# Kernel optimization log

Hardware: AMD Instinct MI355X
Metric: run time of the kernel (lower is better)

The kernel has to match this reference:

```python
import jax, jax.numpy as jnp
import numpy as np

DIM = 1024
HEADS = 16
HD = DIM // HEADS            # 64
MLP = 4 * DIM                # 4096
IN_OUT = MLP + 3 * DIM       # 7168, in_proj out dim
OUT_IN = MLP + DIM           # 5120, out_proj in dim
OUT_OUT = 2 * DIM            # 2048, out_proj out dim
R = 2                        # residual PQ levels
K = 64                       # codebook size
NCB = HEADS                  # num_codebooks = num_heads * codebooks_ratio
IN_CLUSTERS = HEADS * (IN_OUT // DIM)                 # 112
OUT_CLUSTERS = HEADS * max(1, OUT_OUT // OUT_IN)      # 16
SUB_IN = DIM // NCB          # 64
SUB_OUT = OUT_IN // NCB      # 320
EPS = 1e-5


def setup_inputs() -> dict:
    key = jax.random.key(0)
    k1, k2, k3, k4, k5 = jax.random.split(key, 5)
    B, N = 4, 1024
    x = jax.random.normal(k1, (B, N, DIM), jnp.float32)
    in_codebooks = jax.random.normal(k2, (R, IN_CLUSTERS, NCB, K, SUB_IN), jnp.float32) * 0.02
    in_indices = jax.random.randint(k3, (R, IN_OUT, NCB), 0, K, jnp.int32)
    out_codebooks = jax.random.normal(k4, (R, OUT_CLUSTERS, NCB, K, SUB_OUT), jnp.float32) * 0.02
    out_indices = jax.random.randint(k5, (R, OUT_OUT, NCB), 0, K, jnp.int32)
    return {"x": x, "in_codebooks": in_codebooks, "in_indices": in_indices,
            "out_codebooks": out_codebooks, "out_indices": out_indices}


def _decode_weight(cb, idx):
    """Decode RPQ weight. cb: (R, n_clusters, n_codebooks, K, sub), idx: (R, O, n_codebooks).
    Returns dense weight (O, n_codebooks*sub)."""
    Rr, nclust, C, _, sub = cb.shape
    O = idx.shape[1]
    cluster = jnp.arange(O) // (O // nclust)                       # per-row cluster id
    w = cb[jnp.arange(Rr)[:, None, None],
           cluster[None, :, None],
           jnp.arange(C)[None, None, :],
           idx]                                                    # (R, O, C, sub)
    return w.sum(0).reshape(O, C * sub)


def reference(x, in_codebooks, in_indices, out_codebooks, out_indices):
    B, N, C = x.shape
    res = x
    # LayerNorm without affine
    mu = x.mean(-1, keepdims=True)
    var = x.var(-1, keepdims=True)
    xn = (x - mu) * jax.lax.rsqrt(var + EPS)
    # in_proj: dequant + GEMM
    Win = _decode_weight(in_codebooks, in_indices)                 # (IN_OUT, DIM)
    h = jnp.einsum('bnc,oc->bno', xn, Win)                         # (B, N, IN_OUT)
    xm, q, k, v = jnp.split(h, [MLP, MLP + DIM, MLP + 2 * DIM], axis=-1)
    q = q.reshape(B, N, HEADS, HD).transpose(0, 2, 1, 3)
    k = k.reshape(B, N, HEADS, HD).transpose(0, 2, 1, 3)
    v = v.reshape(B, N, HEADS, HD).transpose(0, 2, 1, 3)
    scale = HD ** -0.5
    attn = jax.nn.softmax(jnp.einsum('bhqd,bhkd->bhqk', q, k) * scale, axis=-1)
    xa = jnp.einsum('bhqk,bhkd->bhqd', attn, v).transpose(0, 2, 1, 3).reshape(B, N, C)
    # out_proj: dequant + GEMM on concatenated [mlp, attn]
    Wout = _decode_weight(out_codebooks, out_indices)              # (OUT_OUT, OUT_IN)
    o = jnp.einsum('bnc,oc->bno', jnp.concatenate([xm, xa], axis=-1), Wout)
    x_mlp, x_attn = o[..., :DIM], o[..., DIM:]
    return x_mlp + x_attn + res
```

## Files before the change

kernel.cpp:

```cpp
#include <hip/hip_runtime.h>
#include <hip/hip_bf16.h>

typedef float f32x4 __attribute__((ext_vector_type(4)));
typedef short short8 __attribute__((ext_vector_type(8)));

#define LDH 7168
#define MFMA16(d, x, y) d = __builtin_amdgcn_mfma_f32_16x16x32_bf16(x, y, d, 0, 0, 0)

__device__ __forceinline__ void async_ld16(const void* g, void* l) {
  __builtin_amdgcn_global_load_lds(
      (const __attribute__((address_space(1))) unsigned int*)g,
      (__attribute__((address_space(3))) unsigned int*)l, 16, 0, 0);
}

__device__ __forceinline__ float bf2f(unsigned short u) {
  union { unsigned int i; float f; } c; c.i = ((unsigned int)u) << 16; return c.f;
}

__device__ __forceinline__ ushort4 pack_bf16x4(float4 v) {
  ushort4 u;
  __hip_bfloat16 b;
  b = __float2bfloat16(v.x); u.x = *(unsigned short*)&b;
  b = __float2bfloat16(v.y); u.y = *(unsigned short*)&b;
  b = __float2bfloat16(v.z); u.z = *(unsigned short*)&b;
  b = __float2bfloat16(v.w); u.w = *(unsigned short*)&b;
  return u;
}

__global__ __launch_bounds__(256) void decode_win_k(const float* __restrict__ cb,
                                                    const int* __restrict__ idx,
                                                    __hip_bfloat16* __restrict__ Win) {
  const int o = blockIdx.x;
  const int cluster = o >> 6;
  const int c = threadIdx.x >> 4;
  const int s4 = (threadIdx.x & 15) * 4;
  const int k0 = idx[o * 16 + c];
  const int k1 = idx[(7168 + o) * 16 + c];
  const float4 v0 = *(const float4*)&cb[((((size_t)cluster) * 16 + c) * 64 + k0) * 64 + s4];
  const float4 v1 = *(const float4*)&cb[((((size_t)(112 + cluster)) * 16 + c) * 64 + k1) * 64 + s4];
  float4 v; v.x = v0.x + v1.x; v.y = v0.y + v1.y; v.z = v0.z + v1.z; v.w = v0.w + v1.w;
  *(ushort4*)&Win[(size_t)o * 1024 + c * 64 + s4] = pack_bf16x4(v);
}

__global__ __launch_bounds__(256) void decode_weff_k(const float* __restrict__ cb,
                                                     const int* __restrict__ idx,
                                                     __hip_bfloat16* __restrict__ W) {
  const int o = blockIdx.x;
  const int cl1 = o >> 7, cl2 = cl1 + 8;
  for (int e4 = threadIdx.x * 4; e4 < 5120; e4 += 1024) {
    const int c = e4 / 320, s = e4 - c * 320;
    float4 acc = {0.f, 0.f, 0.f, 0.f};
    #pragma unroll
    for (int r = 0; r < 2; ++r) {
      const int ka = idx[((size_t)r * 2048 + o) * 16 + c];
      const int kb = idx[((size_t)r * 2048 + o + 1024) * 16 + c];
      const float4 va = *(const float4*)&cb[((((size_t)r * 16 + cl1) * 16 + c) * 64 + ka) * 320 + s];
      const float4 vb = *(const float4*)&cb[((((size_t)r * 16 + cl2) * 16 + c) * 64 + kb) * 320 + s];
      acc.x += va.x + vb.x; acc.y += va.y + vb.y; acc.z += va.z + vb.z; acc.w += va.w + vb.w;
    }
    *(ushort4*)&W[(size_t)o * 5120 + e4] = pack_bf16x4(acc);
  }
}

__global__ __launch_bounds__(256) void ln_k(const float* __restrict__ x,
                                            __hip_bfloat16* __restrict__ xn) {
  const int row = blockIdx.x;
  const float4 v = ((const float4*)(x + (size_t)row * 1024))[threadIdx.x];
  float s = v.x + v.y + v.z + v.w;
  float s2 = v.x * v.x + v.y * v.y + v.z * v.z + v.w * v.w;
  #pragma unroll
  for (int off = 32; off > 0; off >>= 1) {
    s += __shfl_down(s, off, 64);
    s2 += __shfl_down(s2, off, 64);
  }
  __shared__ float red[8];
  if ((threadIdx.x & 63) == 0) { red[threadIdx.x >> 6] = s; red[4 + (threadIdx.x >> 6)] = s2; }
  __syncthreads();
  s = red[0] + red[1] + red[2] + red[3];
  s2 = red[4] + red[5] + red[6] + red[7];
  const float mu = s * (1.f / 1024.f);
  const float rstd = rsqrtf(s2 * (1.f / 1024.f) - mu * mu + 1e-5f);
  float4 nv;
  nv.x = (v.x - mu) * rstd; nv.y = (v.y - mu) * rstd;
  nv.z = (v.z - mu) * rstd; nv.w = (v.w - mu) * rstd;
  *(ushort4*)(xn + (size_t)row * 1024 + threadIdx.x * 4) = pack_bf16x4(nv);
}

__global__ __launch_bounds__(512, 2) void gemm1_k(const __hip_bfloat16* __restrict__ A,
                                                  const __hip_bfloat16* __restrict__ B,
                                                  __hip_bfloat16* __restrict__ C,
                                                  __hip_bfloat16* __restrict__ vT) {
  __shared__ ushort sm[65536];
  const int tid = threadIdx.x;
  const int lane = tid & 63, wid = tid >> 6;
  const int g = lane >> 4, r16 = lane & 15;
  const int wr = wid >> 2, wc = wid & 3;

  const int x = blockIdx.x & 7, local = blockIdx.x >> 3;
  const int mb = (x >> 1) * 4 + local / 14;
  const int nb = (x & 1) * 14 + local % 14;
  const int m0 = mb * 256, n0 = nb * 256;

  auto stageA = [&](int kt, int base) {
    #pragma unroll
    for (int i = 0; i < 4; ++i) {
      const int c = i * 512 + tid;
      const int lc = c ^ (((c >> 5) & 1) << 1);
      const int row = lc >> 3, col = (lc & 7) * 8;
      async_ld16(&A[(size_t)(m0 + row) * 1024 + kt * 64 + col], &sm[base + c * 8]);
    }
  };
  auto stageB = [&](int kt, int base) {
    #pragma unroll
    for (int i = 0; i < 4; ++i) {
      const int c = i * 512 + tid;
      const int lc = c ^ (((c >> 5) & 1) << 1);
      const int row = lc >> 3, col = (lc & 7) * 8;
      async_ld16(&B[(size_t)(n0 + row) * 1024 + kt * 64 + col], &sm[base + 16384 + c * 8]);
    }
  };
  auto rdA = [&](int base, int mm, int kk) -> short8 {
    const int row = wr * 128 + mm * 16 + r16;
    int e = row * 64 + kk * 32 + g * 8;
    e ^= ((row >> 2) & 1) << 4;
    return *(const short8*)&sm[base + e];
  };
  auto rdB = [&](int base, int nn, int kk) -> short8 {
    const int row = wc * 64 + nn * 16 + r16;
    int e = row * 64 + kk * 32 + g * 8;
    e ^= ((row >> 2) & 1) << 4;
    return *(const short8*)&sm[base + 16384 + e];
  };

  f32x4 acc[8][4] = {};

  stageA(0, 0); stageB(0, 0);
  asm volatile("s_waitcnt vmcnt(0)" ::: "memory");
  __builtin_amdgcn_s_barrier();
  __builtin_amdgcn_sched_barrier(0);

  auto tile_body = [&](int kt, int base, int nbase) {
    short8 a0[4][2], a1[4][2], b0[2][2], b1[2][2];
    #pragma unroll
    for (int mm = 0; mm < 4; ++mm) { a0[mm][0] = rdA(base, mm, 0); a0[mm][1] = rdA(base, mm, 1); }
    #pragma unroll
    for (int nn = 0; nn < 2; ++nn) { b0[nn][0] = rdB(base, nn, 0); b0[nn][1] = rdB(base, nn, 1); }
    if (kt + 1 < 16) stageA(kt + 1, nbase);
    __builtin_amdgcn_s_setprio(1);
    #pragma unroll
    for (int mm = 0; mm < 4; ++mm)
      #pragma unroll
      for (int nn = 0; nn < 2; ++nn) {
        MFMA16(acc[mm][nn], a0[mm][0], b0[nn][0]);
        MFMA16(acc[mm][nn], a0[mm][1], b0[nn][1]);
      }
    __builtin_amdgcn_s_setprio(0);
    __builtin_amdgcn_s_barrier();
    #pragma unroll
    for (int nn = 0; nn < 2; ++nn) { b1[nn][0] = rdB(base, 2 + nn, 0); b1[nn][1] = rdB(base, 2 + nn, 1); }
    if (kt + 1 < 16) stageB(kt + 1, nbase);
    __builtin_amdgcn_s_setprio(1);
    #pragma unroll
    for (int mm = 0; mm < 4; ++mm)
      #pragma unroll
      for (int nn = 0; nn < 2; ++nn) {
        MFMA16(acc[mm][2 + nn], a0[mm][0], b1[nn][0]);
        MFMA16(acc[mm][2 + nn], a0[mm][1], b1[nn][1]);
      }
    __builtin_amdgcn_s_setprio(0);
    __builtin_amdgcn_s_barrier();
    #pragma unroll
    for (int mm = 0; mm < 4; ++mm) { a1[mm][0] = rdA(base, 4 + mm, 0); a1[mm][1] = rdA(base, 4 + mm, 1); }
    __builtin_amdgcn_s_setprio(1);
    #pragma unroll
    for (int mm = 0; mm < 4; ++mm)
      #pragma unroll
      for (int nn = 0; nn < 2; ++nn) {
        MFMA16(acc[4 + mm][2 + nn], a1[mm][0], b1[nn][0]);
        MFMA16(acc[4 + mm][2 + nn], a1[mm][1], b1[nn][1]);
      }
    __builtin_amdgcn_s_setprio(0);
    __builtin_amdgcn_s_barrier();
    __builtin_amdgcn_s_setprio(1);
    #pragma unroll
    for (int mm = 0; mm < 4; ++mm)
      #pragma unroll
      for (int nn = 0; nn < 2; ++nn) {
        MFMA16(acc[4 + mm][nn], a1[mm][0], b0[nn][0]);
        MFMA16(acc[4 + mm][nn], a1[mm][1], b0[nn][1]);
      }
    __builtin_amdgcn_s_setprio(0);
    asm volatile("s_waitcnt vmcnt(0) lgkmcnt(0)" ::: "memory");
    __builtin_amdgcn_s_barrier();
    __builtin_amdgcn_sched_barrier(0);
  };

  for (int kt = 0; kt < 16; kt += 2) {
    tile_body(kt, 0, 32768);
    tile_body(kt + 1, 32768, 0);
  }

  if (n0 < 6144) {
    #pragma unroll
    for (int mm = 0; mm < 8; ++mm)
      #pragma unroll
      for (int nn = 0; nn < 4; ++nn)
        #pragma unroll
        for (int r = 0; r < 4; ++r) {
          const int m = m0 + wr * 128 + mm * 16 + g * 4 + r;
          const int o = n0 + wc * 64 + nn * 16 + r16;
          C[(size_t)m * LDH + o] = __float2bfloat16(acc[mm][nn][r]);
        }
  } else {
    #pragma unroll
    for (int mm = 0; mm < 8; ++mm)
      #pragma unroll
      for (int nn = 0; nn < 4; ++nn)
        #pragma unroll
        for (int r = 0; r < 4; ++r) {
          const int m = m0 + wr * 128 + mm * 16 + g * 4 + r;
          const int o = n0 + wc * 64 + nn * 16 + r16;
          const int b_ = m >> 10;
          vT[((size_t)b_ * 1024 + (o - 6144)) * 1024 + (m & 1023)] = __float2bfloat16(acc[mm][nn][r]);
        }
  }
}

__global__ __launch_bounds__(256) void attn_k(const __hip_bfloat16* __restrict__ h,
                                              const __hip_bfloat16* __restrict__ vT,
                                              __hip_bfloat16* __restrict__ xa) {
  const int qt = blockIdx.x, head = blockIdx.y, b = blockIdx.z;
  const int tid = threadIdx.x;
  const int lane = tid & 63, w = tid >> 6;
  const int g = lane >> 4, r16 = lane & 15;

  __shared__ __align__(16) __hip_bfloat16 Ks[2][64 * 64];
  __shared__ __align__(16) __hip_bfloat16 Vs[2][64 * 64];
  __shared__ __align__(16) __hip_bfloat16 P[4][16][72];

  const __hip_bfloat16* Kg = h + (size_t)(b * 1024) * LDH + 5120 + head * 64;
  const __hip_bfloat16* Vg = vT + ((size_t)b * 1024 + head * 64) * 1024;

  const size_t qrow = (size_t)(b * 1024 + qt * 64 + w * 16 + r16);
  short8 aq0 = *(const short8*)&h[qrow * LDH + 4096 + head * 64 + g * 8];
  short8 aq1 = *(const short8*)&h[qrow * LDH + 4096 + head * 64 + 32 + g * 8];

  auto stage = [&](int buf, int t) {
    #pragma unroll
    for (int i = 0; i < 2; ++i) {
      const int c_lin = i * 256 + tid;
      const int row = c_lin >> 3;
      const int c_log = (c_lin & 7) ^ (row & 7);
      async_ld16(&Kg[(size_t)(t * 64 + row) * LDH + c_log * 8], &Ks[buf][c_lin * 8]);
    }
    #pragma unroll
    for (int i = 0; i < 2; ++i) {
      const int c_lin = i * 256 + tid;
      const int row = c_lin >> 3;
      const int c_log = (c_lin & 7) ^ (row & 7);
      async_ld16(&Vg[(size_t)row * 1024 + t * 64 + c_log * 8], &Vs[buf][c_lin * 8]);
    }
  };

  f32x4 o_acc[4] = {};
  float m_r[4], l_r[4];
  #pragma unroll
  for (int r = 0; r < 4; ++r) { m_r[r] = -1e30f; l_r[r] = 0.f; }

  stage(0, 0);
  for (int t = 0; t < 16; ++t) {
    const int buf = t & 1;
    if (t + 1 < 16) {
      stage(buf ^ 1, t + 1);
      asm volatile("s_waitcnt vmcnt(4)" ::: "memory");
    } else {
      asm volatile("s_waitcnt vmcnt(0)" ::: "memory");
    }
    __builtin_amdgcn_s_barrier();
    __builtin_amdgcn_sched_barrier(0);

    f32x4 s_acc[4] = {};
    #pragma unroll
    for (int nn = 0; nn < 4; ++nn) {
      const int row = nn * 16 + r16;
      short8 bk0 = *(const short8*)&Ks[buf][row * 64 + ((g ^ (row & 7)) * 8)];
      short8 bk1 = *(const short8*)&Ks[buf][row * 64 + (((g + 4) ^ (row & 7)) * 8)];
      s_acc[nn] = __builtin_amdgcn_mfma_f32_16x16x32_bf16(aq0, bk0, s_acc[nn], 0, 0, 0);
      s_acc[nn] = __builtin_amdgcn_mfma_f32_16x16x32_bf16(aq1, bk1, s_acc[nn], 0, 0, 0);
    }
    #pragma unroll
    for (int nn = 0; nn < 4; ++nn) s_acc[nn] *= 0.125f;

    #pragma unroll
    for (int r = 0; r < 4; ++r) {
      float mx = fmaxf(fmaxf(s_acc[0][r], s_acc[1][r]), fmaxf(s_acc[2][r], s_acc[3][r]));
      #pragma unroll
      for (int off = 1; off < 16; off <<= 1) mx = fmaxf(mx, __shfl_xor(mx, off, 64));
      const float mn = fmaxf(m_r[r], mx);
      const float al = __expf(m_r[r] - mn);
      m_r[r] = mn;
      float ps = 0.f;
      #pragma unroll
      for (int nn = 0; nn < 4; ++nn) {
        const float p = __expf(s_acc[nn][r] - mn);
        s_acc[nn][r] = p;
        ps += p;
      }
      #pragma unroll
      for (int off = 1; off < 16; off <<= 1) ps += __shfl_xor(ps, off, 64);
      l_r[r] = l_r[r] * al + ps;
      o_acc[0][r] *= al; o_acc[1][r] *= al; o_acc[2][r] *= al; o_acc[3][r] *= al;
    }

    #pragma unroll
    for (int nn = 0; nn < 4; ++nn)
      #pragma unroll
      for (int r = 0; r < 4; ++r)
        P[w][g * 4 + r][nn * 16 + r16] = __float2bfloat16(s_acc[nn][r]);
    short8 ap0 = *(const short8*)&P[w][r16][g * 8];
    short8 ap1 = *(const short8*)&P[w][r16][32 + g * 8];

    #pragma unroll
    for (int nn = 0; nn < 4; ++nn) {
      const int row = nn * 16 + r16;
      short8 bv0 = *(const short8*)&Vs[buf][row * 64 + ((g ^ (row & 7)) * 8)];
      short8 bv1 = *(const short8*)&Vs[buf][row * 64 + (((g + 4) ^ (row & 7)) * 8)];
      o_acc[nn] = __builtin_amdgcn_mfma_f32_16x16x32_bf16(ap0, bv0, o_acc[nn], 0, 0, 0);
      o_acc[nn] = __builtin_amdgcn_mfma_f32_16x16x32_bf16(ap1, bv1, o_acc[nn], 0, 0, 0);
    }
    __builtin_amdgcn_s_barrier();
    __builtin_amdgcn_sched_barrier(0);
  }

  #pragma unroll
  for (int r = 0; r < 4; ++r) {
    const float inv = 1.0f / l_r[r];
    const size_t mrow = (size_t)(b * 1024 + qt * 64 + w * 16 + g * 4 + r);
    #pragma unroll
    for (int nn = 0; nn < 4; ++nn)
      xa[mrow * 1024 + head * 64 + nn * 16 + r16] = __float2bfloat16(o_acc[nn][r] * inv);
  }
}

__global__ __launch_bounds__(512, 2) void gemm2_k(const __hip_bfloat16* __restrict__ h,
                                                  const __hip_bfloat16* __restrict__ xa,
                                                  const __hip_bfloat16* __restrict__ W,
                                                  __hip_bfloat16* __restrict__ p0,
                                                  __hip_bfloat16* __restrict__ p1,
                                                  __hip_bfloat16* __restrict__ p2,
                                                  float* __restrict__ out) {
  __shared__ ushort sm[65536];
  const int tid = threadIdx.x;
  const int lane = tid & 63, wid = tid >> 6;
  const int g = lane >> 4, r16 = lane & 15;
  const int wr = wid >> 2, wc = wid & 3;

  int bid = blockIdx.x;
  bid = (bid & 7) * 8 + (bid >> 3);
  const int mb = bid >> 2, nb = bid & 3;
  const int m0 = mb * 256, n0 = nb * 256;
  const int z = blockIdx.y;
  const int kt0 = z * 20, ktEnd = kt0 + 20;

  auto stageA = [&](int kt, int base) {
    const __hip_bfloat16* Ab; size_t lda; int kc;
    if (kt < 64) { Ab = h;  lda = LDH;  kc = kt * 64; }
    else         { Ab = xa; lda = 1024; kc = kt * 64 - 4096; }
    #pragma unroll
    for (int i = 0; i < 4; ++i) {
      const int c = i * 512 + tid;
      const int lc = c ^ (((c >> 5) & 1) << 1);
      const int row = lc >> 3, col = (lc & 7) * 8;
      async_ld16(&Ab[(size_t)(m0 + row) * lda + kc + col], &sm[base + c * 8]);
    }
  };
  auto stageB = [&](int kt, int base) {
    #pragma unroll
    for (int i = 0; i < 4; ++i) {
      const int c = i * 512 + tid;
      const int lc = c ^ (((c >> 5) & 1) << 1);
      const int row = lc >> 3, col = (lc & 7) * 8;
      async_ld16(&W[(size_t)(n0 + row) * 5120 + kt * 64 + col], &sm[base + 16384 + c * 8]);
    }
  };
  auto rdA = [&](int base, int mm, int kk) -> short8 {
    const int row = wr * 128 + mm * 16 + r16;
    int e = row * 64 + kk * 32 + g * 8;
    e ^= ((row >> 2) & 1) << 4;
    return *(const short8*)&sm[base + e];
  };
  auto rdB = [&](int base, int nn, int kk) -> short8 {
    const int row = wc * 64 + nn * 16 + r16;
    int e = row * 64 + kk * 32 + g * 8;
    e ^= ((row >> 2) & 1) << 4;
    return *(const short8*)&sm[base + 16384 + e];
  };

  f32x4 acc[8][4] = {};

  stageA(kt0, 0); stageB(kt0, 0);
  asm volatile("s_waitcnt vmcnt(0)" ::: "memory");
  __builtin_amdgcn_s_barrier();
  __builtin_amdgcn_sched_barrier(0);

  auto tile_body = [&](int kt, int base, int nbase) {
    short8 a0[4][2], a1[4][2], b0[2][2], b1[2][2];
    #pragma unroll
    for (int mm = 0; mm < 4; ++mm) { a0[mm][0] = rdA(base, mm, 0); a0[mm][1] = rdA(base, mm, 1); }
    #pragma unroll
    for (int nn = 0; nn < 2; ++nn) { b0[nn][0] = rdB(base, nn, 0); b0[nn][1] = rdB(base, nn, 1); }
    if (kt + 1 < ktEnd) stageA(kt + 1, nbase);
    __builtin_amdgcn_s_setprio(1);
    #pragma unroll
    for (int mm = 0; mm < 4; ++mm)
      #pragma unroll
      for (int nn = 0; nn < 2; ++nn) {
        MFMA16(acc[mm][nn], a0[mm][0], b0[nn][0]);
        MFMA16(acc[mm][nn], a0[mm][1], b0[nn][1]);
      }
    __builtin_amdgcn_s_setprio(0);
    __builtin_amdgcn_s_barrier();
    #pragma unroll
    for (int nn = 0; nn < 2; ++nn) { b1[nn][0] = rdB(base, 2 + nn, 0); b1[nn][1] = rdB(base, 2 + nn, 1); }
    if (kt + 1 < ktEnd) stageB(kt + 1, nbase);
    __builtin_amdgcn_s_setprio(1);
    #pragma unroll
    for (int mm = 0; mm < 4; ++mm)
      #pragma unroll
      for (int nn = 0; nn < 2; ++nn) {
        MFMA16(acc[mm][2 + nn], a0[mm][0], b1[nn][0]);
        MFMA16(acc[mm][2 + nn], a0[mm][1], b1[nn][1]);
      }
    __builtin_amdgcn_s_setprio(0);
    __builtin_amdgcn_s_barrier();
    #pragma unroll
    for (int mm = 0; mm < 4; ++mm) { a1[mm][0] = rdA(base, 4 + mm, 0); a1[mm][1] = rdA(base, 4 + mm, 1); }
    __builtin_amdgcn_s_setprio(1);
    #pragma unroll
    for (int mm = 0; mm < 4; ++mm)
      #pragma unroll
      for (int nn = 0; nn < 2; ++nn) {
        MFMA16(acc[4 + mm][2 + nn], a1[mm][0], b1[nn][0]);
        MFMA16(acc[4 + mm][2 + nn], a1[mm][1], b1[nn][1]);
      }
    __builtin_amdgcn_s_setprio(0);
    __builtin_amdgcn_s_barrier();
    __builtin_amdgcn_s_setprio(1);
    #pragma unroll
    for (int mm = 0; mm < 4; ++mm)
      #pragma unroll
      for (int nn = 0; nn < 2; ++nn) {
        MFMA16(acc[4 + mm][nn], a1[mm][0], b0[nn][0]);
        MFMA16(acc[4 + mm][nn], a1[mm][1], b0[nn][1]);
      }
    __builtin_amdgcn_s_setprio(0);
    asm volatile("s_waitcnt vmcnt(0) lgkmcnt(0)" ::: "memory");
    __builtin_amdgcn_s_barrier();
    __builtin_amdgcn_sched_barrier(0);
  };

  for (int kt = kt0; kt < ktEnd; kt += 2) {
    tile_body(kt, 0, 32768);
    tile_body(kt + 1, 32768, 0);
  }

  __hip_bfloat16* pz = (z == 0) ? p0 : (z == 1) ? p1 : p2;
  #pragma unroll
  for (int mm = 0; mm < 8; ++mm)
    #pragma unroll
    for (int nn = 0; nn < 4; ++nn)
      #pragma unroll
      for (int r = 0; r < 4; ++r) {
        const int m = m0 + wr * 128 + mm * 16 + g * 4 + r;
        const int n = n0 + wc * 64 + nn * 16 + r16;
        if (z == 3) out[(size_t)m * 1024 + n] = acc[mm][nn][r];
        else        pz[(size_t)m * 1024 + n] = __float2bfloat16(acc[mm][nn][r]);
      }
}

__global__ __launch_bounds__(256) void reduce_k(const __hip_bfloat16* __restrict__ p0,
                                                const __hip_bfloat16* __restrict__ p1,
                                                const __hip_bfloat16* __restrict__ p2,
                                                const float* __restrict__ res,
                                                float* __restrict__ out) {
  const size_t i4 = (size_t)blockIdx.x * 256 + threadIdx.x;
  float4 o = ((const float4*)out)[i4];
  const float4 rr = ((const float4*)res)[i4];
  const ushort4 a0 = ((const ushort4*)p0)[i4];
  const ushort4 a1 = ((const ushort4*)p1)[i4];
  const ushort4 a2 = ((const ushort4*)p2)[i4];
  o.x += rr.x + bf2f(a0.x) + bf2f(a1.x) + bf2f(a2.x);
  o.y += rr.y + bf2f(a0.y) + bf2f(a1.y) + bf2f(a2.y);
  o.z += rr.z + bf2f(a0.z) + bf2f(a1.z) + bf2f(a2.z);
  o.w += rr.w + bf2f(a0.w) + bf2f(a1.w) + bf2f(a2.w);
  ((float4*)out)[i4] = o;
}

extern "C" void kernel_launch(void* const* d_in, const int* in_sizes, int n_in,
                              void* d_out, int out_size, void* d_ws, size_t ws_size,
                              hipStream_t stream) {
  (void)in_sizes; (void)n_in; (void)out_size; (void)ws_size;
  const float* x      = (const float*)d_in[0];
  const float* in_cb  = (const float*)d_in[1];
  const int*   in_idx = (const int*)d_in[2];
  const float* out_cb = (const float*)d_in[3];
  const int*   out_idx= (const int*)d_in[4];
  float* out = (float*)d_out;
  char* ws = (char*)d_ws;

  __hip_bfloat16* Win  = (__hip_bfloat16*)(ws);
  __hip_bfloat16* Weff = (__hip_bfloat16*)(ws + 14680064);
  __hip_bfloat16* xn   = (__hip_bfloat16*)(ws + 25165824);
  __hip_bfloat16* h    = (__hip_bfloat16*)(ws + 33554432);
  __hip_bfloat16* vT   = (__hip_bfloat16*)(ws + 92274688);
  __hip_bfloat16* xa   = (__hip_bfloat16*)(ws + 100663296);

  __hip_bfloat16* pk0 = Win;
  __hip_bfloat16* pk1 = xn;
  __hip_bfloat16* pk2 = vT;

  decode_win_k<<<dim3(7168), dim3(256), 0, stream>>>(in_cb, in_idx, Win);
  decode_weff_k<<<dim3(1024), dim3(256), 0, stream>>>(out_cb, out_idx, Weff);
  ln_k<<<dim3(4096), dim3(256), 0, stream>>>(x, xn);
  gemm1_k<<<dim3(448), dim3(512), 0, stream>>>(xn, Win, h, vT);
  attn_k<<<dim3(16, 16, 4), dim3(256), 0, stream>>>(h, vT, xa);
  gemm2_k<<<dim3(64, 4), dim3(512), 0, stream>>>(h, xa, Weff, pk0, pk1, pk2, out);
  reduce_k<<<dim3(4096), dim3(256), 0, stream>>>(pk0, pk1, pk2, x, out);
}
```

Measured before the change: 219.2 us.

## Deepen GEMM prefetch to two tiles ahead with split half-tile async loads

Measured after the change: 220.7 us. Within noise of the previous version (+0.7%).

```diff
diff --git a/kernel.cpp b/kernel.cpp
--- a/kernel.cpp
+++ b/kernel.cpp
@@ -101,22 +101,22 @@
   const int nb = (x & 1) * 14 + local % 14;
   const int m0 = mb * 256, n0 = nb * 256;
 
-  auto stageA = [&](int kt, int base) {
-    #pragma unroll
-    for (int i = 0; i < 4; ++i) {
-      const int c = i * 512 + tid;
+  auto stA = [&](int tt, int hf) {
+    #pragma unroll
+    for (int i = 0; i < 2; ++i) {
+      const int c = hf * 1024 + i * 512 + tid;
       const int lc = c ^ (((c >> 5) & 1) << 1);
       const int row = lc >> 3, col = (lc & 7) * 8;
-      async_ld16(&A[(size_t)(m0 + row) * 1024 + kt * 64 + col], &sm[base + c * 8]);
-    }
-  };
-  auto stageB = [&](int kt, int base) {
-    #pragma unroll
-    for (int i = 0; i < 4; ++i) {
-      const int c = i * 512 + tid;
+      async_ld16(&A[(size_t)(m0 + row) * 1024 + tt * 64 + col], &sm[(tt & 1) * 32768 + c * 8]);
+    }
+  };
+  auto stB = [&](int tt, int hf) {
+    #pragma unroll
+    for (int i = 0; i < 2; ++i) {
+      const int c = hf * 1024 + i * 512 + tid;
       const int lc = c ^ (((c >> 5) & 1) << 1);
       const int row = lc >> 3, col = (lc & 7) * 8;
-      async_ld16(&B[(size_t)(n0 + row) * 1024 + kt * 64 + col], &sm[base + 16384 + c * 8]);
+      async_ld16(&B[(size_t)(n0 + row) * 1024 + tt * 64 + col], &sm[(tt & 1) * 32768 + 16384 + c * 8]);
     }
   };
   auto rdA = [&](int base, int mm, int kk) -> short8 {
@@ -134,18 +134,21 @@
 
   f32x4 acc[8][4] = {};
 
-  stageA(0, 0); stageB(0, 0);
-  asm volatile("s_waitcnt vmcnt(0)" ::: "memory");
+  stA(0, 0); stA(0, 1); stB(0, 0); stB(0, 1);
+  stA(1, 0); stA(1, 1); stB(1, 0); stB(1, 1);
+  asm volatile("s_waitcnt vmcnt(8)" ::: "memory");
   __builtin_amdgcn_s_barrier();
   __builtin_amdgcn_sched_barrier(0);
 
-  auto tile_body = [&](int kt, int base, int nbase) {
+  #pragma unroll 2
+  for (int t = 0; t < 16; ++t) {
+    const int base = (t & 1) * 32768;
     short8 a0[4][2], a1[4][2], b0[2][2], b1[2][2];
     #pragma unroll
     for (int mm = 0; mm < 4; ++mm) { a0[mm][0] = rdA(base, mm, 0); a0[mm][1] = rdA(base, mm, 1); }
     #pragma unroll
     for (int nn = 0; nn < 2; ++nn) { b0[nn][0] = rdB(base, nn, 0); b0[nn][1] = rdB(base, nn, 1); }
-    if (kt + 1 < 16) stageA(kt + 1, nbase);
+    if (t >= 1 && t + 1 < 16) stA(t + 1, 1);
     __builtin_amdgcn_s_setprio(1);
     #pragma unroll
     for (int mm = 0; mm < 4; ++mm)
@@ -156,9 +159,9 @@
       }
     __builtin_amdgcn_s_setprio(0);
     __builtin_amdgcn_s_barrier();
+    __builtin_amdgcn_sched_barrier(0);
     #pragma unroll
     for (int nn = 0; nn < 2; ++nn) { b1[nn][0] = rdB(base, 2 + nn, 0); b1[nn][1] = rdB(base, 2 + nn, 1); }
-    if (kt + 1 < 16) stageB(kt + 1, nbase);
     __builtin_amdgcn_s_setprio(1);
     #pragma unroll
     for (int mm = 0; mm < 4; ++mm)
@@ -169,8 +172,10 @@
       }
     __builtin_amdgcn_s_setprio(0);
     __builtin_amdgcn_s_barrier();
+    __builtin_amdgcn_sched_barrier(0);
     #pragma unroll
     for (int mm = 0; mm < 4; ++mm) { a1[mm][0] = rdA(base, 4 + mm, 0); a1[mm][1] = rdA(base, 4 + mm, 1); }
+    if (t + 2 < 16) stB(t + 2, 0);
     __builtin_amdgcn_s_setprio(1);
     #pragma unroll
     for (int mm = 0; mm < 4; ++mm)
@@ -181,6 +186,8 @@
       }
     __builtin_amdgcn_s_setprio(0);
     __builtin_amdgcn_s_barrier();
+    __builtin_amdgcn_sched_barrier(0);
+    if (t + 2 < 16) { stB(t + 2, 1); stA(t + 2, 0); }
     __builtin_amdgcn_s_setprio(1);
     #pragma unroll
     for (int mm = 0; mm < 4; ++mm)
@@ -190,14 +197,10 @@
         MFMA16(acc[4 + mm][nn], a1[mm][1], b0[nn][1]);
       }
     __builtin_amdgcn_s_setprio(0);
-    asm volatile("s_waitcnt vmcnt(0) lgkmcnt(0)" ::: "memory");
-    __builtin_amdgcn_s_barrier();
-    __builtin_amdgcn_sched_barrier(0);
-  };
-
-  for (int kt = 0; kt < 16; kt += 2) {
-    tile_body(kt, 0, 32768);
-    tile_body(kt + 1, 32768, 0);
+    if (t + 2 < 16) asm volatile("s_waitcnt vmcnt(6)" ::: "memory");
+    else            asm volatile("s_waitcnt vmcnt(0)" ::: "memory");
+    __builtin_amdgcn_s_barrier();
+    __builtin_amdgcn_sched_barrier(0);
   }
 
   if (n0 < 6144) {
@@ -342,7 +345,7 @@
   }
 }
 
-__global__ __launch_bounds__(512, 2) void gemm2_k(const __hip_bfloat16* __restrict__ h,
+__global__ __launch_bounds__(512, 2) void gemm2_k(const __hip_bfloat16* __restrict__ hbuf,
                                                   const __hip_bfloat16* __restrict__ xa,
                                                   const __hip_bfloat16* __restrict__ W,
                                                   __hip_bfloat16* __restrict__ p0,
@@ -360,27 +363,29 @@
   const int mb = bid >> 2, nb = bid & 3;
   const int m0 = mb * 256, n0 = nb * 256;
   const int z = blockIdx.y;
-  const int kt0 = z * 20, ktEnd = kt0 + 20;
-
-  auto stageA = [&](int kt, int base) {
+  const int kt0 = z * 20;
+
+  auto stA = [&](int lt, int hf) {
+    const int gt = kt0 + lt;
     const __hip_bfloat16* Ab; size_t lda; int kc;
-    if (kt < 64) { Ab = h;  lda = LDH;  kc = kt * 64; }
-    else         { Ab = xa; lda = 1024; kc = kt * 64 - 4096; }
-    #pragma unroll
-    for (int i = 0; i < 4; ++i) {
-      const int c = i * 512 + tid;
+    if (gt < 64) { Ab = hbuf; lda = LDH;  kc = gt * 64; }
+    else         { Ab = xa;   lda = 1024; kc = gt * 64 - 4096; }
+    #pragma unroll
+    for (int i = 0; i < 2; ++i) {
+      const int c = hf * 1024 + i * 512 + tid;
       const int lc = c ^ (((c >> 5) & 1) << 1);
       const int row = lc >> 3, col = (lc & 7) * 8;
-      async_ld16(&Ab[(size_t)(m0 + row) * lda + kc + col], &sm[base + c * 8]);
-    }
-  };
-  auto stageB = [&](int kt, int base) {
-    #pragma unroll
-    for (int i = 0; i < 4; ++i) {
-      const int c = i * 512 + tid;
+      async_ld16(&Ab[(size_t)(m0 + row) * lda + kc + col], &sm[(lt & 1) * 32768 + c * 8]);
+    }
+  };
+  auto stB = [&](int lt, int hf) {
+    const int gt = kt0 + lt;
+    #pragma unroll
+    for (int i = 0; i < 2; ++i) {
+      const int c = hf * 1024 + i * 512 + tid;
       const int lc = c ^ (((c >> 5) & 1) << 1);
       const int row = lc >> 3, col = (lc & 7) * 8;
-      async_ld16(&W[(size_t)(n0 + row) * 5120 + kt * 64 + col], &sm[base + 16384 + c * 8]);
+      async_ld16(&W[(size_t)(n0 + row) * 5120 + gt * 64 + col], &sm[(lt & 1) * 32768 + 16384 + c * 8]);
     }
   };
   auto rdA = [&](int base, int mm, int kk) -> short8 {
@@ -398,18 +403,21 @@
 
   f32x4 acc[8][4] = {};
 
-  stageA(kt0, 0); stageB(kt0, 0);
-  asm volatile("s_waitcnt vmcnt(0)" ::: "memory");
+  stA(0, 0); stA(0, 1); stB(0, 0); stB(0, 1);
+  stA(1, 0); stA(1, 1); stB(1, 0); stB(1, 1);
+  asm volatile("s_waitcnt vmcnt(8)" ::: "memory");
   __builtin_amdgcn_s_barrier();
   __builtin_amdgcn_sched_barrier(0);
 
-  auto tile_body = [&](int kt, int base, int nbase) {
+  #pragma unroll 2
+  for (int t = 0; t < 20; ++t) {
+    const int base = (t & 1) * 32768;
     short8 a0[4][2], a1[4][2], b0[2][2], b1[2][2];
     #pragma unroll
     for (int mm = 0; mm < 4; ++mm) { a0[mm][0] = rdA(base, mm, 0); a0[mm][1] = rdA(base, mm, 1); }
     #pragma unroll
     for (int nn = 0; nn < 2; ++nn) { b0[nn][0] = rdB(base, nn, 0); b0[nn][1] = rdB(base, nn, 1); }
-    if (kt + 1 < ktEnd) stageA(kt + 1, nbase);
+    if (t >= 1 && t + 1 < 20) stA(t + 1, 1);
     __builtin_amdgcn_s_setprio(1);
     #pragma unroll
     for (int mm = 0; mm < 4; ++mm)
@@ -420,9 +428,9 @@
       }
     __builtin_amdgcn_s_setprio(0);
     __builtin_amdgcn_s_barrier();
+    __builtin_amdgcn_sched_barrier(0);
     #pragma unroll
     for (int nn = 0; nn < 2; ++nn) { b1[nn][0] = rdB(base, 2 + nn, 0); b1[nn][1] = rdB(base, 2 + nn, 1); }
-    if (kt + 1 < ktEnd) stageB(kt + 1, nbase);
     __builtin_amdgcn_s_setprio(1);
     #pragma unroll
     for (int mm = 0; mm < 4; ++mm)
@@ -433,8 +441,10 @@
       }
     __builtin_amdgcn_s_setprio(0);
     __builtin_amdgcn_s_barrier();
+    __builtin_amdgcn_sched_barrier(0);
     #pragma unroll
     for (int mm = 0; mm < 4; ++mm) { a1[mm][0] = rdA(base, 4 + mm, 0); a1[mm][1] = rdA(base, 4 + mm, 1); }
+    if (t + 2 < 20) stB(t + 2, 0);
     __builtin_amdgcn_s_setprio(1);
     #pragma unroll
     for (int mm = 0; mm < 4; ++mm)
@@ -445,6 +455,8 @@
       }
     __builtin_amdgcn_s_setprio(0);
     __builtin_amdgcn_s_barrier();
+    __builtin_amdgcn_sched_barrier(0);
+    if (t + 2 < 20) { stB(t + 2, 1); stA(t + 2, 0); }
     __builtin_amdgcn_s_setprio(1);
     #pragma unroll
     for (int mm = 0; mm < 4; ++mm)
@@ -454,14 +466,10 @@
         MFMA16(acc[4 + mm][nn], a1[mm][1], b0[nn][1]);
       }
     __builtin_amdgcn_s_setprio(0);
-    asm volatile("s_waitcnt vmcnt(0) lgkmcnt(0)" ::: "memory");
-    __builtin_amdgcn_s_barrier();
-    __builtin_amdgcn_sched_barrier(0);
-  };
-
-  for (int kt = kt0; kt < ktEnd; kt += 2) {
-    tile_body(kt, 0, 32768);
-    tile_body(kt + 1, 32768, 0);
+    if (t + 2 < 20) asm volatile("s_waitcnt vmcnt(6)" ::: "memory");
+    else            asm volatile("s_waitcnt vmcnt(0)" ::: "memory");
+    __builtin_amdgcn_s_barrier();
+    __builtin_amdgcn_sched_barrier(0);
   }
 
   __hip_bfloat16* pz = (z == 0) ? p0 : (z == 1) ? p1 : p2;
```

## Process two query tiles per attention block and fold residual into gemm2 epilogue

Applied to the files above, without the earlier changes.

Result: slower. 249.4 us (+13.8%).

```diff
diff --git a/kernel.cpp b/kernel.cpp
--- a/kernel.cpp
+++ b/kernel.cpp
@@ -229,7 +229,7 @@
 __global__ __launch_bounds__(256) void attn_k(const __hip_bfloat16* __restrict__ h,
                                               const __hip_bfloat16* __restrict__ vT,
                                               __hip_bfloat16* __restrict__ xa) {
-  const int qt = blockIdx.x, head = blockIdx.y, b = blockIdx.z;
+  const int qtp = blockIdx.x, head = blockIdx.y, b = blockIdx.z;
   const int tid = threadIdx.x;
   const int lane = tid & 63, w = tid >> 6;
   const int g = lane >> 4, r16 = lane & 15;
@@ -241,9 +241,13 @@
   const __hip_bfloat16* Kg = h + (size_t)(b * 1024) * LDH + 5120 + head * 64;
   const __hip_bfloat16* Vg = vT + ((size_t)b * 1024 + head * 64) * 1024;
 
-  const size_t qrow = (size_t)(b * 1024 + qt * 64 + w * 16 + r16);
-  short8 aq0 = *(const short8*)&h[qrow * LDH + 4096 + head * 64 + g * 8];
-  short8 aq1 = *(const short8*)&h[qrow * LDH + 4096 + head * 64 + 32 + g * 8];
+  short8 aq[2][2];
+  #pragma unroll
+  for (int qs = 0; qs < 2; ++qs) {
+    const size_t qrow = (size_t)(b * 1024 + qtp * 128 + qs * 64 + w * 16 + r16);
+    aq[qs][0] = *(const short8*)&h[qrow * LDH + 4096 + head * 64 + g * 8];
+    aq[qs][1] = *(const short8*)&h[qrow * LDH + 4096 + head * 64 + 32 + g * 8];
+  }
 
   auto stage = [&](int buf, int t) {
     #pragma unroll
@@ -262,10 +266,12 @@
     }
   };
 
-  f32x4 o_acc[4] = {};
-  float m_r[4], l_r[4];
+  f32x4 o_acc[2][4] = {};
+  float m_r[2][4], l_r[2][4];
   #pragma unroll
-  for (int r = 0; r < 4; ++r) { m_r[r] = -1e30f; l_r[r] = 0.f; }
+  for (int qs = 0; qs < 2; ++qs)
+    #pragma unroll
+    for (int r = 0; r < 4; ++r) { m_r[qs][r] = -1e30f; l_r[qs][r] = 0.f; }
 
   stage(0, 0);
   for (int t = 0; t < 16; ++t) {
@@ -279,72 +285,78 @@
     __builtin_amdgcn_s_barrier();
     __builtin_amdgcn_sched_barrier(0);
 
-    f32x4 s_acc[4] = {};
-    #pragma unroll
-    for (int nn = 0; nn < 4; ++nn) {
-      const int row = nn * 16 + r16;
-      short8 bk0 = *(const short8*)&Ks[buf][row * 64 + ((g ^ (row & 7)) * 8)];
-      short8 bk1 = *(const short8*)&Ks[buf][row * 64 + (((g + 4) ^ (row & 7)) * 8)];
-      s_acc[nn] = __builtin_amdgcn_mfma_f32_16x16x32_bf16(aq0, bk0, s_acc[nn], 0, 0, 0);
-      s_acc[nn] = __builtin_amdgcn_mfma_f32_16x16x32_bf16(aq1, bk1, s_acc[nn], 0, 0, 0);
-    }
-    #pragma unroll
-    for (int nn = 0; nn < 4; ++nn) s_acc[nn] *= 0.125f;
-
+    #pragma unroll
+    for (int qs = 0; qs < 2; ++qs) {
+      f32x4 s_acc[4] = {};
+      #pragma unroll
+      for (int nn = 0; nn < 4; ++nn) {
+        const int row = nn * 16 + r16;
+        short8 bk0 = *(const short8*)&Ks[buf][row * 64 + ((g ^ (row & 7)) * 8)];
+        short8 bk1 = *(const short8*)&Ks[buf][row * 64 + (((g + 4) ^ (row & 7)) * 8)];
+        s_acc[nn] = __builtin_amdgcn_mfma_f32_16x16x32_bf16(aq[qs][0], bk0, s_acc[nn], 0, 0, 0);
+        s_acc[nn] = __builtin_amdgcn_mfma_f32_16x16x32_bf16(aq[qs][1], bk1, s_acc[nn], 0, 0, 0);
+      }
+      #pragma unroll
+      for (int nn = 0; nn < 4; ++nn) s_acc[nn] *= 0.125f;
+
+      #pragma unroll
+      for (int r = 0; r < 4; ++r) {
+        float mx = fmaxf(fmaxf(s_acc[0][r], s_acc[1][r]), fmaxf(s_acc[2][r], s_acc[3][r]));
+        #pragma unroll
+        for (int off = 1; off < 16; off <<= 1) mx = fmaxf(mx, __shfl_xor(mx, off, 64));
+        const float mn = fmaxf(m_r[qs][r], mx);
+        const float al = __expf(m_r[qs][r] - mn);
+        m_r[qs][r] = mn;
+        float ps = 0.f;
+        #pragma unroll
+        for (int nn = 0; nn < 4; ++nn) {
+          const float p = __expf(s_acc[nn][r] - mn);
+          s_acc[nn][r] = p;
+          ps += p;
+        }
+        #pragma unroll
+        for (int off = 1; off < 16; off <<= 1) ps += __shfl_xor(ps, off, 64);
+        l_r[qs][r] = l_r[qs][r] * al + ps;
+        o_acc[qs][0][r] *= al; o_acc[qs][1][r] *= al; o_acc[qs][2][r] *= al; o_acc[qs][3][r] *= al;
+      }
+
+      #pragma unroll
+      for (int nn = 0; nn < 4; ++nn)
+        #pragma unroll
+        for (int r = 0; r < 4; ++r)
+          P[w][g * 4 + r][nn * 16 + r16] = __float2bfloat16(s_acc[nn][r]);
+      short8 ap0 = *(const short8*)&P[w][r16][g * 8];
+      short8 ap1 = *(const short8*)&P[w][r16][32 + g * 8];
+
+      #pragma unroll
+      for (int nn = 0; nn < 4; ++nn) {
+        const int row = nn * 16 + r16;
+        short8 bv0 = *(const short8*)&Vs[buf][row * 64 + ((g ^ (row & 7)) * 8)];
+        short8 bv1 = *(const short8*)&Vs[buf][row * 64 + (((g + 4) ^ (row & 7)) * 8)];
+        o_acc[qs][nn] = __builtin_amdgcn_mfma_f32_16x16x32_bf16(ap0, bv0, o_acc[qs][nn], 0, 0, 0);
+        o_acc[qs][nn] = __builtin_amdgcn_mfma_f32_16x16x32_bf16(ap1, bv1, o_acc[qs][nn], 0, 0, 0);
+      }
+    }
+    __builtin_amdgcn_s_barrier();
+    __builtin_amdgcn_sched_barrier(0);
+  }
+
+  #pragma unroll
+  for (int qs = 0; qs < 2; ++qs)
     #pragma unroll
     for (int r = 0; r < 4; ++r) {
-      float mx = fmaxf(fmaxf(s_acc[0][r], s_acc[1][r]), fmaxf(s_acc[2][r], s_acc[3][r]));
-      #pragma unroll
-      for (int off = 1; off < 16; off <<= 1) mx = fmaxf(mx, __shfl_xor(mx, off, 64));
-      const float mn = fmaxf(m_r[r], mx);
-      const float al = __expf(m_r[r] - mn);
-      m_r[r] = mn;
-      float ps = 0.f;
-      #pragma unroll
-      for (int nn = 0; nn < 4; ++nn) {
-        const float p = __expf(s_acc[nn][r] - mn);
-        s_acc[nn][r] = p;
-        ps += p;
-      }
-      #pragma unroll
-      for (int off = 1; off < 16; off <<= 1) ps += __shfl_xor(ps, off, 64);
-      l_r[r] = l_r[r] * al + ps;
-      o_acc[0][r] *= al; o_acc[1][r] *= al; o_acc[2][r] *= al; o_acc[3][r] *= al;
-    }
-
-    #pragma unroll
-    for (int nn = 0; nn < 4; ++nn)
-      #pragma unroll
-      for (int r = 0; r < 4; ++r)
-        P[w][g * 4 + r][nn * 16 + r16] = __float2bfloat16(s_acc[nn][r]);
-    short8 ap0 = *(const short8*)&P[w][r16][g * 8];
-    short8 ap1 = *(const short8*)&P[w][r16][32 + g * 8];
-
-    #pragma unroll
-    for (int nn = 0; nn < 4; ++nn) {
-      const int row = nn * 16 + r16;
-      short8 bv0 = *(const short8*)&Vs[buf][row * 64 + ((g ^ (row & 7)) * 8)];
-      short8 bv1 = *(const short8*)&Vs[buf][row * 64 + (((g + 4) ^ (row & 7)) * 8)];
-      o_acc[nn] = __builtin_amdgcn_mfma_f32_16x16x32_bf16(ap0, bv0, o_acc[nn], 0, 0, 0);
-      o_acc[nn] = __builtin_amdgcn_mfma_f32_16x16x32_bf16(ap1, bv1, o_acc[nn], 0, 0, 0);
-    }
-    __builtin_amdgcn_s_barrier();
-    __builtin_amdgcn_sched_barrier(0);
-  }
-
-  #pragma unroll
-  for (int r = 0; r < 4; ++r) {
-    const float inv = 1.0f / l_r[r];
-    const size_t mrow = (size_t)(b * 1024 + qt * 64 + w * 16 + g * 4 + r);
-    #pragma unroll
-    for (int nn = 0; nn < 4; ++nn)
-      xa[mrow * 1024 + head * 64 + nn * 16 + r16] = __float2bfloat16(o_acc[nn][r] * inv);
-  }
+      const float inv = 1.0f / l_r[qs][r];
+      const size_t mrow = (size_t)(b * 1024 + qtp * 128 + qs * 64 + w * 16 + g * 4 + r);
+      #pragma unroll
+      for (int nn = 0; nn < 4; ++nn)
+        xa[mrow * 1024 + head * 64 + nn * 16 + r16] = __float2bfloat16(o_acc[qs][nn][r] * inv);
+    }
 }
 
 __global__ __launch_bounds__(512, 2) void gemm2_k(const __hip_bfloat16* __restrict__ h,
                                                   const __hip_bfloat16* __restrict__ xa,
                                                   const __hip_bfloat16* __restrict__ W,
+                                                  const float* __restrict__ res,
                                                   __hip_bfloat16* __restrict__ p0,
                                                   __hip_bfloat16* __restrict__ p1,
                                                   __hip_bfloat16* __restrict__ p2,
@@ -473,7 +485,7 @@
       for (int r = 0; r < 4; ++r) {
         const int m = m0 + wr * 128 + mm * 16 + g * 4 + r;
         const int n = n0 + wc * 64 + nn * 16 + r16;
-        if (z == 3) out[(size_t)m * 1024 + n] = acc[mm][nn][r];
+        if (z == 3) out[(size_t)m * 1024 + n] = acc[mm][nn][r] + res[(size_t)m * 1024 + n];
         else        pz[(size_t)m * 1024 + n] = __float2bfloat16(acc[mm][nn][r]);
       }
 }
@@ -481,18 +493,16 @@
 __global__ __launch_bounds__(256) void reduce_k(const __hip_bfloat16* __restrict__ p0,
                                                 const __hip_bfloat16* __restrict__ p1,
                                                 const __hip_bfloat16* __restrict__ p2,
-                                                const float* __restrict__ res,
                                                 float* __restrict__ out) {
   const size_t i4 = (size_t)blockIdx.x * 256 + threadIdx.x;
   float4 o = ((const float4*)out)[i4];
-  const float4 rr = ((const float4*)res)[i4];
   const ushort4 a0 = ((const ushort4*)p0)[i4];
   const ushort4 a1 = ((const ushort4*)p1)[i4];
   const ushort4 a2 = ((const ushort4*)p2)[i4];
-  o.x += rr.x + bf2f(a0.x) + bf2f(a1.x) + bf2f(a2.x);
-  o.y += rr.y + bf2f(a0.y) + bf2f(a1.y) + bf2f(a2.y);
-  o.z += rr.z + bf2f(a0.z) + bf2f(a1.z) + bf2f(a2.z);
-  o.w += rr.w + bf2f(a0.w) + bf2f(a1.w) + bf2f(a2.w);
+  o.x += bf2f(a0.x) + bf2f(a1.x) + bf2f(a2.x);
+  o.y += bf2f(a0.y) + bf2f(a1.y) + bf2f(a2.y);
+  o.z += bf2f(a0.z) + bf2f(a1.z) + bf2f(a2.z);
+  o.w += bf2f(a0.w) + bf2f(a1.w) + bf2f(a2.w);
   ((float4*)out)[i4] = o;
 }
 
@@ -523,7 +533,7 @@
   decode_weff_k<<<dim3(1024), dim3(256), 0, stream>>>(out_cb, out_idx, Weff);
   ln_k<<<dim3(4096), dim3(256), 0, stream>>>(x, xn);
   gemm1_k<<<dim3(448), dim3(512), 0, stream>>>(xn, Win, h, vT);
-  attn_k<<<dim3(16, 16, 4), dim3(256), 0, stream>>>(h, vT, xa);
-  gemm2_k<<<dim3(64, 4), dim3(512), 0, stream>>>(h, xa, Weff, pk0, pk1, pk2, out);
-  reduce_k<<<dim3(4096), dim3(256), 0, stream>>>(pk0, pk1, pk2, x, out);
-}
+  attn_k<<<dim3(8, 16, 4), dim3(256), 0, stream>>>(h, vT, xa);
+  gemm2_k<<<dim3(64, 4), dim3(512), 0, stream>>>(h, xa, Weff, x, pk0, pk1, pk2, out);
+  reduce_k<<<dim3(4096), dim3(256), 0, stream>>>(pk0, pk1, pk2, out);
+}
```
